# Performance work log

Hardware: AMD Instinct MI355X
Metric: run time of the kernel (lower is better)

Reference implementation:

```python
import jax, jax.numpy as jnp
import numpy as np

N, E, D_IN, D_OUT = 16384, 4096, 256, 256


def _leaky(v):
    return jnp.where(v > 0, v, 0.1 * v)


def setup_inputs() -> dict:
    key = jax.random.key(0)
    ks = jax.random.split(key, 8)
    x = jax.random.normal(ks[0], (N, D_IN), dtype=jnp.float32)
    # 0/1 incidence mask, float32 (as multiplied in the torch code)
    H_shape = jax.random.randint(ks[1], (N, E), 0, 2).astype(jnp.float32)
    w1 = jax.random.normal(ks[2], (D_IN, D_OUT), dtype=jnp.float32)
    w2 = jax.random.normal(ks[3], (D_OUT, D_OUT), dtype=jnp.float32)
    a1 = jax.random.normal(ks[4], (D_OUT, 1), dtype=jnp.float32)
    a21 = jax.random.normal(ks[5], (D_OUT, 1), dtype=jnp.float32)
    a22 = jax.random.normal(ks[6], (D_OUT, 1), dtype=jnp.float32)
    return {"x": x, "H_shape": H_shape, "w1": w1, "w2": w2,
            "a1": a1, "a21": a21, "a22": a22}


def reference(x, H_shape, w1, w2, a1, a21, a22):
    xw1 = x @ w1                                  # [N, D]
    # node->edge attention (masked softmax-like over nodes, axis -2)
    f = _leaky(xw1) @ a1                          # [N, 1]
    e = jnp.exp(jnp.tanh(f / 8) * 8) * H_shape    # [N, E]
    e = e / jnp.sum(e, axis=-2, keepdims=True)    # normalize over nodes
    # edge features
    f = _leaky(e.T @ xw1)                         # [E, D]
    # edge->node attention (masked normalize over edges, axis -1)
    b = (_leaky(f @ w2) @ a21).T + _leaky(xw1) @ a22  # [1,E] + [N,1] -> [N,E]
    b = jnp.exp(jnp.tanh(b / 8) * 8) * H_shape
    b = b / jnp.sum(b, axis=-1, keepdims=True)
    return _leaky(b @ f @ w2)                     # [N, D]
```

## Files before the change

### kernel.cpp

```cpp
#include <hip/hip_runtime.h>


typedef __attribute__((ext_vector_type(8))) short short8;
typedef __attribute__((ext_vector_type(4))) short short4v;
typedef __attribute__((ext_vector_type(4))) float f32x4;

__device__ __forceinline__ float leakyf(float v) { return v > 0.f ? v : 0.1f * v; }
__device__ __forceinline__ float fastrcp(float x) { return __builtin_amdgcn_rcpf(x); }

__device__ __forceinline__ float satexpf(float t) {
    float u = fminf(fmaxf(t * 0.25f, -30.f), 30.f);
    float p = __expf(u);
    float th = (p - 1.f) * fastrcp(p + 1.f);
    return __expf(8.f * th);
}

__device__ __forceinline__ short f2b(float v) {
    unsigned int x = __float_as_uint(v);
    x += 0x7fffu + ((x >> 16) & 1u);
    return (short)(x >> 16);
}
__device__ __forceinline__ float b2f(short s) {
    return __uint_as_float(((unsigned int)(unsigned short)s) << 16);
}

__global__ __launch_bounds__(256) void transpose_f32_bf16(
        const float* __restrict__ src, short* __restrict__ dst, int R, int C) {
    __shared__ float Ts[64][65];
    const int t = threadIdx.x;
    const long r0 = (long)blockIdx.x * 64;
    const long c0 = (long)blockIdx.y * 64;
    {
        const int row = t >> 2, cc = (t & 3) * 16;
        const float* p = src + (r0 + row) * (long)C + c0 + cc;
#pragma unroll
        for (int i = 0; i < 4; ++i) {
            f32x4 v = *reinterpret_cast<const f32x4*>(p + i * 4);
#pragma unroll
            for (int k = 0; k < 4; ++k) Ts[row][cc + i * 4 + k] = v[k];
        }
    }
    __syncthreads();
    {
        const int cl = t >> 2, ch = (t & 3) * 16;
        short8 pk0, pk1;
#pragma unroll
        for (int i = 0; i < 8; ++i) pk0[i] = f2b(Ts[ch + i][cl]);
#pragma unroll
        for (int i = 0; i < 8; ++i) pk1[i] = f2b(Ts[ch + 8 + i][cl]);
        short* q = dst + (c0 + cl) * (long)R + r0 + ch;
        *reinterpret_cast<short8*>(q) = pk0;
        *reinterpret_cast<short8*>(q + 8) = pk1;
    }
}

__global__ __launch_bounds__(256) void transpose_split(
        const float* __restrict__ src, short* __restrict__ dh,
        short* __restrict__ dl, int R, int C) {
    __shared__ float Ts[64][65];
    const int t = threadIdx.x;
    const long r0 = (long)blockIdx.x * 64;
    const long c0 = (long)blockIdx.y * 64;
    {
        const int row = t >> 2, cc = (t & 3) * 16;
        const float* p = src + (r0 + row) * (long)C + c0 + cc;
#pragma unroll
        for (int i = 0; i < 4; ++i) {
            f32x4 v = *reinterpret_cast<const f32x4*>(p + i * 4);
#pragma unroll
            for (int k = 0; k < 4; ++k) Ts[row][cc + i * 4 + k] = v[k];
        }
    }
    __syncthreads();
    {
        const int cl = t >> 2, ch = (t & 3) * 16;
        short8 h0, h1, l0, l1;
#pragma unroll
        for (int i = 0; i < 8; ++i) {
            float v = Ts[ch + i][cl];
            short h = f2b(v);
            h0[i] = h; l0[i] = f2b(v - b2f(h));
        }
#pragma unroll
        for (int i = 0; i < 8; ++i) {
            float v = Ts[ch + 8 + i][cl];
            short h = f2b(v);
            h1[i] = h; l1[i] = f2b(v - b2f(h));
        }
        short* qh = dh + (c0 + cl) * (long)R + r0 + ch;
        short* ql = dl + (c0 + cl) * (long)R + r0 + ch;
        *reinterpret_cast<short8*>(qh) = h0;
        *reinterpret_cast<short8*>(qh + 8) = h1;
        *reinterpret_cast<short8*>(ql) = l0;
        *reinterpret_cast<short8*>(ql + 8) = l1;
    }
}

__global__ __launch_bounds__(256) void gemm_xw1(
        const float* __restrict__ A, const short* __restrict__ Bh,
        const short* __restrict__ Bl, float* __restrict__ C) {
    __shared__ short Ash[128][72];
    __shared__ short Asl[128][72];
    __shared__ short Bsh[64][72];
    __shared__ short Bsl[64][72];
    const int t = threadIdx.x;
    const int wid = t >> 6, lane = t & 63;
    const int wm = wid & 1, wn = wid >> 1;
    const int quad = lane >> 4, l15 = lane & 15;
    const long m0 = (long)blockIdx.x * 128;
    const long n0 = (long)blockIdx.y * 64;
    f32x4 acc[4][2];
#pragma unroll
    for (int i = 0; i < 4; ++i)
#pragma unroll
        for (int j = 0; j < 2; ++j)
#pragma unroll
            for (int r = 0; r < 4; ++r) acc[i][j][r] = 0.f;

    for (int kb = 0; kb < 256; kb += 64) {
#pragma unroll
        for (int it = 0; it < 4; ++it) {
            const int cid = t + it * 256;
            const int row = cid >> 3, c8 = (cid & 7) * 8;
            const float* ap = A + (m0 + row) * 256 + kb + c8;
            f32x4 v0 = *reinterpret_cast<const f32x4*>(ap);
            f32x4 v1 = *reinterpret_cast<const f32x4*>(ap + 4);
            short8 hi, lo;
#pragma unroll
            for (int k = 0; k < 4; ++k) {
                short h0 = f2b(v0[k]); hi[k] = h0; lo[k] = f2b(v0[k] - b2f(h0));
                short h1 = f2b(v1[k]); hi[4 + k] = h1; lo[4 + k] = f2b(v1[k] - b2f(h1));
            }
            *reinterpret_cast<short8*>(&Ash[row][c8]) = hi;
            *reinterpret_cast<short8*>(&Asl[row][c8]) = lo;
        }
#pragma unroll
        for (int it = 0; it < 2; ++it) {
            const int cid = t + it * 256;
            const int row = cid >> 3, c8 = (cid & 7) * 8;
            *reinterpret_cast<short8*>(&Bsh[row][c8]) =
                *reinterpret_cast<const short8*>(Bh + (n0 + row) * 256 + kb + c8);
            *reinterpret_cast<short8*>(&Bsl[row][c8]) =
                *reinterpret_cast<const short8*>(Bl + (n0 + row) * 256 + kb + c8);
        }
        __syncthreads();
#pragma unroll
        for (int ks = 0; ks < 2; ++ks) {
            short8 ah[4], al[4], bh[2], bl[2];
#pragma unroll
            for (int i = 0; i < 4; ++i) {
                ah[i] = *reinterpret_cast<const short8*>(&Ash[wm * 64 + i * 16 + l15][ks * 32 + quad * 8]);
                al[i] = *reinterpret_cast<const short8*>(&Asl[wm * 64 + i * 16 + l15][ks * 32 + quad * 8]);
            }
#pragma unroll
            for (int j = 0; j < 2; ++j) {
                bh[j] = *reinterpret_cast<const short8*>(&Bsh[wn * 32 + j * 16 + l15][ks * 32 + quad * 8]);
                bl[j] = *reinterpret_cast<const short8*>(&Bsl[wn * 32 + j * 16 + l15][ks * 32 + quad * 8]);
            }
#pragma unroll
            for (int i = 0; i < 4; ++i)
#pragma unroll
                for (int j = 0; j < 2; ++j) {
                    acc[i][j] = __builtin_amdgcn_mfma_f32_16x16x32_bf16(ah[i], bh[j], acc[i][j], 0, 0, 0);
                    acc[i][j] = __builtin_amdgcn_mfma_f32_16x16x32_bf16(ah[i], bl[j], acc[i][j], 0, 0, 0);
                    acc[i][j] = __builtin_amdgcn_mfma_f32_16x16x32_bf16(al[i], bh[j], acc[i][j], 0, 0, 0);
                }
        }
        __syncthreads();
    }
#pragma unroll
    for (int i = 0; i < 4; ++i) {
        const long grow = m0 + wm * 64 + i * 16 + quad * 4;
#pragma unroll
        for (int j = 0; j < 2; ++j) {
            const long gcol = n0 + wn * 32 + j * 16 + l15;
#pragma unroll
            for (int r = 0; r < 4; ++r)
                C[(grow + r) * 256 + gcol] = acc[i][j][r];
        }
    }
}

__global__ __launch_bounds__(256) void node_stats(
        const float* __restrict__ xw1, const float* __restrict__ a1,
        const float* __restrict__ a22, short* __restrict__ yT,
        float* __restrict__ dn) {
    __shared__ short Ys[257][72];
    const int t = threadIdx.x;
    const int n0 = blockIdx.x * 64;
    const int r = t >> 2, q = t & 3;
    const long n = n0 + r;
    const float* xp = xw1 + n * 256 + q * 64;
    float vals[64];
    float facc = 0.f, dacc = 0.f;
#pragma unroll
    for (int i = 0; i < 16; ++i) {
        f32x4 v  = *reinterpret_cast<const f32x4*>(xp + i * 4);
        f32x4 b1 = *reinterpret_cast<const f32x4*>(a1 + q * 64 + i * 4);
        f32x4 b2 = *reinterpret_cast<const f32x4*>(a22 + q * 64 + i * 4);
#pragma unroll
        for (int k = 0; k < 4; ++k) {
            float lv = leakyf(v[k]);
            facc += lv * b1[k];
            dacc += lv * b2[k];
            vals[i * 4 + k] = v[k];
        }
    }
    facc += __shfl_xor(facc, 1); facc += __shfl_xor(facc, 2);
    dacc += __shfl_xor(dacc, 1); dacc += __shfl_xor(dacc, 2);
    const float g = satexpf(facc);
    const int dr = t >> 3, c8 = (t & 7) * 8;
    if (q == 0) { dn[n] = dacc; Ys[256][r] = f2b(g); }
#pragma unroll
    for (int i = 0; i < 64; ++i) Ys[q * 64 + i][r] = f2b(vals[i] * g);
    __syncthreads();
    for (int it = 0; it < 9; ++it) {
        const int d = it * 32 + dr;
        short8 pk;
        if (d <= 256) pk = *reinterpret_cast<const short8*>(&Ys[d][c8]);
        else { short8 z = {0,0,0,0,0,0,0,0}; pk = z; }
        *reinterpret_cast<short8*>(yT + (long)d * 16384 + n0 + c8) = pk;
    }
    __syncthreads();
    if (q == 0) Ys[256][r] = f2b(g - b2f(f2b(g)));
#pragma unroll
    for (int i = 0; i < 64; ++i) {
        float yv = vals[i] * g;
        Ys[q * 64 + i][r] = f2b(yv - b2f(f2b(yv)));
    }
    __syncthreads();
    for (int it = 0; it < 9; ++it) {
        const int d = it * 32 + dr;
        short8 pk;
        if (d <= 256) pk = *reinterpret_cast<const short8*>(&Ys[d][c8]);
        else { short8 z = {0,0,0,0,0,0,0,0}; pk = z; }
        *reinterpret_cast<short8*>(yT + (long)(288 + d) * 16384 + n0 + c8) = pk;
    }
}

template<int BM, int BN, int EPI>
__global__ __launch_bounds__(256) void gemm_bt(
        const short* __restrict__ Ab, const short* __restrict__ Bb,
        float* __restrict__ C, long ldA, long ldB, long ldC,
        int Ktile, const float* __restrict__ aux, long zstrideC) {
    constexpr int BK = 64;
    constexpr int TM = BM / 32, TN = BN / 32;
    __shared__ short As[BM][BK + 8];
    __shared__ short Bs[BN][BK + 8];
    const int t = threadIdx.x;
    const int wid = t >> 6, lane = t & 63;
    const int wm = wid & 1, wn = wid >> 1;
    const int quad = lane >> 4, l15 = lane & 15;
    const long m0 = (long)blockIdx.x * BM;
    const long n0 = (long)blockIdx.y * BN;
    const long k0 = (long)blockIdx.z * Ktile;
    float* Cz = C + (long)blockIdx.z * zstrideC;

    f32x4 acc[TM][TN];
#pragma unroll
    for (int i = 0; i < TM; ++i)
#pragma unroll
        for (int j = 0; j < TN; ++j)
#pragma unroll
            for (int r = 0; r < 4; ++r) acc[i][j][r] = 0.f;

    for (int kb = 0; kb < Ktile; kb += BK) {
#pragma unroll
        for (int it = 0; it < BM * BK / 2048; ++it) {
            const int cid = t + it * 256;
            const int row = cid >> 3, c8 = (cid & 7) * 8;
            *reinterpret_cast<short8*>(&As[row][c8]) =
                *reinterpret_cast<const short8*>(Ab + (m0 + row) * ldA + k0 + kb + c8);
        }
#pragma unroll
        for (int it = 0; it < BN * BK / 2048; ++it) {
            const int cid = t + it * 256;
            const int row = cid >> 3, c8 = (cid & 7) * 8;
            *reinterpret_cast<short8*>(&Bs[row][c8]) =
                *reinterpret_cast<const short8*>(Bb + (n0 + row) * ldB + k0 + kb + c8);
        }
        __syncthreads();
#pragma unroll
        for (int ks = 0; ks < 2; ++ks) {
            short8 af[TM], bf[TN];
#pragma unroll
            for (int i = 0; i < TM; ++i)
                af[i] = *reinterpret_cast<const short8*>(
                        &As[wm * (BM / 2) + i * 16 + l15][ks * 32 + quad * 8]);
#pragma unroll
            for (int j = 0; j < TN; ++j)
                bf[j] = *reinterpret_cast<const short8*>(
                        &Bs[wn * (BN / 2) + j * 16 + l15][ks * 32 + quad * 8]);
#pragma unroll
            for (int i = 0; i < TM; ++i)
#pragma unroll
                for (int j = 0; j < TN; ++j)
                    acc[i][j] = __builtin_amdgcn_mfma_f32_16x16x32_bf16(
                            af[i], bf[j], acc[i][j], 0, 0, 0);
        }
        __syncthreads();
    }
#pragma unroll
    for (int i = 0; i < TM; ++i) {
        const long grow = m0 + wm * (BM / 2) + i * 16 + quad * 4;
#pragma unroll
        for (int j = 0; j < TN; ++j) {
            const long gcol = n0 + wn * (BN / 2) + j * 16 + l15;
#pragma unroll
            for (int r = 0; r < 4; ++r) {
                const float v = acc[i][j][r];
                float* cp = Cz + (grow + r) * ldC + gcol;
                if (EPI == 0) *cp = v;
                else *cp = leakyf(v * fastrcp(aux[grow + r]));
            }
        }
    }
}

__global__ __launch_bounds__(256) void reduce_C1(
        const float* __restrict__ C1p, float* __restrict__ C1) {
    const int i = blockIdx.x * 256 + threadIdx.x;
    const int j = i / 288, dd = i - j * 288;
    const float* p = C1p + (long)j * 576 + dd;
    float s = 0.f;
#pragma unroll
    for (int z = 0; z < 4; ++z) {
        const float* pz = p + (long)z * 4096 * 576;
        s += pz[0] + pz[288];
    }
    C1[i] = s;
}

__global__ __launch_bounds__(256) void gemm_G(
        const float* __restrict__ C1, const short* __restrict__ w2Th,
        const short* __restrict__ w2Tl, const float* __restrict__ a21,
        short* __restrict__ GT, float* __restrict__ cat) {
    __shared__ short Ash[64][72];
    __shared__ short Asl[64][72];
    __shared__ short Bsh[64][72];
    __shared__ short Bsl[64][72];
    __shared__ float Gs[64][65];
    const int t = threadIdx.x;
    const int wid = t >> 6, lane = t & 63;
    const int wm = wid & 1, wn = wid >> 1;
    const int quad = lane >> 4, l15 = lane & 15;
    const long j0 = (long)blockIdx.x * 64;
    const long d0 = (long)blockIdx.y * 64;
    f32x4 acc[2][2];
#pragma unroll
    for (int i = 0; i < 2; ++i)
#pragma unroll
        for (int j = 0; j < 2; ++j)
#pragma unroll
            for (int r = 0; r < 4; ++r) acc[i][j][r] = 0.f;

    for (int kb = 0; kb < 256; kb += 64) {
#pragma unroll
        for (int it = 0; it < 2; ++it) {
            const int cid = t + it * 256;
            const int row = cid >> 3, c8 = (cid & 7) * 8;
            const float rd = fastrcp(C1[(j0 + row) * 288 + 256]);
            const float* ap = C1 + (j0 + row) * 288 + kb + c8;
            f32x4 v0 = *reinterpret_cast<const f32x4*>(ap);
            f32x4 v1 = *reinterpret_cast<const f32x4*>(ap + 4);
            short8 hi, lo;
#pragma unroll
            for (int k = 0; k < 4; ++k) {
                float f0 = leakyf(v0[k] * rd);
                float f1 = leakyf(v1[k] * rd);
                short h0 = f2b(f0); hi[k] = h0; lo[k] = f2b(f0 - b2f(h0));
                short h1 = f2b(f1); hi[4 + k] = h1; lo[4 + k] = f2b(f1 - b2f(h1));
            }
            *reinterpret_cast<short8*>(&Ash[row][c8]) = hi;
            *reinterpret_cast<short8*>(&Asl[row][c8]) = lo;
            *reinterpret_cast<short8*>(&Bsh[row][c8]) =
                *reinterpret_cast<const short8*>(w2Th + (d0 + row) * 256 + kb + c8);
            *reinterpret_cast<short8*>(&Bsl[row][c8]) =
                *reinterpret_cast<const short8*>(w2Tl + (d0 + row) * 256 + kb + c8);
        }
        __syncthreads();
#pragma unroll
        for (int ks = 0; ks < 2; ++ks) {
            short8 ah[2], al[2], bh[2], bl[2];
#pragma unroll
            for (int i = 0; i < 2; ++i) {
                ah[i] = *reinterpret_cast<const short8*>(&Ash[wm * 32 + i * 16 + l15][ks * 32 + quad * 8]);
                al[i] = *reinterpret_cast<const short8*>(&Asl[wm * 32 + i * 16 + l15][ks * 32 + quad * 8]);
            }
#pragma unroll
            for (int j = 0; j < 2; ++j) {
                bh[j] = *reinterpret_cast<const short8*>(&Bsh[wn * 32 + j * 16 + l15][ks * 32 + quad * 8]);
                bl[j] = *reinterpret_cast<const short8*>(&Bsl[wn * 32 + j * 16 + l15][ks * 32 + quad * 8]);
            }
#pragma unroll
            for (int i = 0; i < 2; ++i)
#pragma unroll
                for (int j = 0; j < 2; ++j) {
                    acc[i][j] = __builtin_amdgcn_mfma_f32_16x16x32_bf16(ah[i], bh[j], acc[i][j], 0, 0, 0);
                    acc[i][j] = __builtin_amdgcn_mfma_f32_16x16x32_bf16(ah[i], bl[j], acc[i][j], 0, 0, 0);
                    acc[i][j] = __builtin_amdgcn_mfma_f32_16x16x32_bf16(al[i], bh[j], acc[i][j], 0, 0, 0);
                }
        }
        __syncthreads();
    }
#pragma unroll
    for (int i = 0; i < 2; ++i)
#pragma unroll
        for (int j = 0; j < 2; ++j)
#pragma unroll
            for (int r = 0; r < 4; ++r)
                Gs[wm * 32 + i * 16 + quad * 4 + r][wn * 32 + j * 16 + l15] = acc[i][j][r];
    __syncthreads();
    {
        const int jl = t >> 2, q = t & 3;
        float cp = 0.f;
#pragma unroll
        for (int i = 0; i < 16; ++i) {
            const int d = q * 16 + i;
            cp += leakyf(Gs[jl][d]) * a21[d0 + d];
        }
        cp += __shfl_xor(cp, 1); cp += __shfl_xor(cp, 2);
        if (q == 0) atomicAdd(&cat[j0 + jl], cp);
    }
    {
        const int dl = t >> 2, q = t & 3;
        short8 pk0, pk1;
#pragma unroll
        for (int i = 0; i < 8; ++i) pk0[i] = f2b(Gs[q * 16 + i][dl]);
#pragma unroll
        for (int i = 0; i < 8; ++i) pk1[i] = f2b(Gs[q * 16 + 8 + i][dl]);
        short* gp = GT + (d0 + dl) * 4096 + j0 + q * 16;
        *reinterpret_cast<short8*>(gp) = pk0;
        *reinterpret_cast<short8*>(gp + 8) = pk1;
    }
}

__global__ __launch_bounds__(256) void edge_weights(
        const float* __restrict__ H, const float* __restrict__ cat,
        const float* __restrict__ dn, short* __restrict__ Bmat,
        float* __restrict__ rsum) {
    const long n = blockIdx.x;
    const int t = threadIdx.x;
    const float dv = dn[n];
    const float* hp = H + n * 4096;
    short* bp = Bmat + n * 4096;
    float acc = 0.f;
#pragma unroll
    for (int c = 0; c < 4; ++c) {
        const int j = c * 1024 + t * 4;
        f32x4 h  = *reinterpret_cast<const f32x4*>(hp + j);
        f32x4 cv = *reinterpret_cast<const f32x4*>(cat + j);
        short4v pk;
#pragma unroll
        for (int k = 0; k < 4; ++k) {
            const float s = satexpf(cv[k] + dv) * h[k];
            const short sb = f2b(s);
            pk[k] = sb;
            acc += b2f(sb);
        }
        *reinterpret_cast<short4v*>(bp + j) = pk;
    }
#pragma unroll
    for (int m = 1; m < 64; m <<= 1) acc += __shfl_xor(acc, m);
    __shared__ float wsum[4];
    if ((t & 63) == 0) wsum[t >> 6] = acc;
    __syncthreads();
    if (t == 0) rsum[n] = wsum[0] + wsum[1] + wsum[2] + wsum[3];
}

extern "C" void kernel_launch(void* const* d_in, const int* in_sizes, int n_in,
                              void* d_out, int out_size, void* d_ws, size_t ws_size,
                              hipStream_t stream) {
    const float* x   = (const float*)d_in[0];
    const float* H   = (const float*)d_in[1];
    const float* w1  = (const float*)d_in[2];
    const float* w2  = (const float*)d_in[3];
    const float* a1  = (const float*)d_in[4];
    const float* a21 = (const float*)d_in[5];
    const float* a22 = (const float*)d_in[6];
    float* out = (float*)d_out;
    char* ws = (char*)d_ws;

    float* xw1  = (float*)(ws + 0);
    float* C1p  = (float*)(ws + 0);
    short* yT   = (short*)(ws + 37748736);
    float* dn   = (float*)(ws + 56623104);
    short* w1Th = (short*)(ws + 56688640);
    short* w1Tl = (short*)(ws + 56819712);
    short* w2Th = (short*)(ws + 56950784);
    short* w2Tl = (short*)(ws + 57081856);
    float* C1   = (float*)(ws + 57212928);
    short* GT   = (short*)(ws + 61931520);
    float* cat  = (float*)(ws + 64028672);
    float* rsum = (float*)(ws + 64045056);
    short* HbT  = (short*)(ws + 64110592);
    short* Bmat = HbT;

    transpose_split<<<dim3(4, 4), 256, 0, stream>>>(w1, w1Th, w1Tl, 256, 256);
    transpose_split<<<dim3(4, 4), 256, 0, stream>>>(w2, w2Th, w2Tl, 256, 256);
    transpose_f32_bf16<<<dim3(256, 64), 256, 0, stream>>>(H, HbT, 16384, 4096);

    gemm_xw1<<<dim3(128, 4), 256, 0, stream>>>(x, w1Th, w1Tl, xw1);

    node_stats<<<dim3(256), 256, 0, stream>>>(xw1, a1, a22, yT, dn);

    gemm_bt<128, 96, 0><<<dim3(32, 6, 4), 256, 0, stream>>>(
            HbT, yT, C1p, 16384, 16384, 576, 4096, nullptr, (long)4096 * 576);
    reduce_C1<<<dim3(4608), 256, 0, stream>>>(C1p, C1);

    hipMemsetAsync(cat, 0, 4096 * sizeof(float), stream);
    gemm_G<<<dim3(64, 4), 256, 0, stream>>>(C1, w2Th, w2Tl, a21, GT, cat);

    edge_weights<<<dim3(16384), 256, 0, stream>>>(H, cat, dn, Bmat, rsum);

    gemm_bt<128, 64, 2><<<dim3(128, 4, 1), 256, 0, stream>>>(
            Bmat, GT, out, 4096, 4096, 256, 4096, rsum, 0);
}
```

Measured before the change: 727.0 us.

## Quantize H·Y GEMM to int8 split hi/lo with per-column scaling, bit-pack H mask

Replaces the bf16 hi/lo split H^T·Y GEMM with an int8 MFMA GEMM. H is exact as an int8 0/1 mask, and Y is quantized into two int8 halves of a 16-bit fixed-point value using per-column max scales gathered with atomicMax. H is also packed into a bitmask so edge_weights reads 1 bit instead of one fp32 per element. The final GEMM moves to a dedicated kernel with a 64x128 tile. This halves operand bytes for the largest GEMM and removes a second full read of H, at the cost of an extra quantization pass, scale atomics, and fixed-point precision loss.

New measurement: 673.3 us. -7.4%, faster.

```diff
diff --git a/kernel.cpp b/kernel.cpp
--- a/kernel.cpp
+++ b/kernel.cpp
@@ -2,8 +2,9 @@
 
 
 typedef __attribute__((ext_vector_type(8))) short short8;
-typedef __attribute__((ext_vector_type(4))) short short4v;
 typedef __attribute__((ext_vector_type(4))) float f32x4;
+typedef __attribute__((ext_vector_type(4))) int int4v;
+typedef __attribute__((ext_vector_type(4))) unsigned int uint4v;
 
 __device__ __forceinline__ float leakyf(float v) { return v > 0.f ? v : 0.1f * v; }
 __device__ __forceinline__ float fastrcp(float x) { return __builtin_amdgcn_rcpf(x); }
@@ -22,36 +23,6 @@
 }
 __device__ __forceinline__ float b2f(short s) {
     return __uint_as_float(((unsigned int)(unsigned short)s) << 16);
-}
-
-__global__ __launch_bounds__(256) void transpose_f32_bf16(
-        const float* __restrict__ src, short* __restrict__ dst, int R, int C) {
-    __shared__ float Ts[64][65];
-    const int t = threadIdx.x;
-    const long r0 = (long)blockIdx.x * 64;
-    const long c0 = (long)blockIdx.y * 64;
-    {
-        const int row = t >> 2, cc = (t & 3) * 16;
-        const float* p = src + (r0 + row) * (long)C + c0 + cc;
-#pragma unroll
-        for (int i = 0; i < 4; ++i) {
-            f32x4 v = *reinterpret_cast<const f32x4*>(p + i * 4);
-#pragma unroll
-            for (int k = 0; k < 4; ++k) Ts[row][cc + i * 4 + k] = v[k];
-        }
-    }
-    __syncthreads();
-    {
-        const int cl = t >> 2, ch = (t & 3) * 16;
-        short8 pk0, pk1;
-#pragma unroll
-        for (int i = 0; i < 8; ++i) pk0[i] = f2b(Ts[ch + i][cl]);
-#pragma unroll
-        for (int i = 0; i < 8; ++i) pk1[i] = f2b(Ts[ch + 8 + i][cl]);
-        short* q = dst + (c0 + cl) * (long)R + r0 + ch;
-        *reinterpret_cast<short8*>(q) = pk0;
-        *reinterpret_cast<short8*>(q + 8) = pk1;
-    }
 }
 
 __global__ __launch_bounds__(256) void transpose_split(
@@ -93,6 +64,47 @@
         *reinterpret_cast<short8*>(qh + 8) = h1;
         *reinterpret_cast<short8*>(ql) = l0;
         *reinterpret_cast<short8*>(ql + 8) = l1;
+    }
+}
+
+__global__ __launch_bounds__(256) void transposeH_pack(
+        const float* __restrict__ H, char* __restrict__ HbT,
+        unsigned int* __restrict__ Hbits) {
+    __shared__ float Ts[64][65];
+    const int t = threadIdx.x;
+    const long r0 = (long)blockIdx.x * 64;
+    const long c0 = (long)blockIdx.y * 64;
+    {
+        const int row = t >> 2, cc = (t & 3) * 16;
+        const float* p = H + (r0 + row) * 4096L + c0 + cc;
+#pragma unroll
+        for (int i = 0; i < 4; ++i) {
+            f32x4 v = *reinterpret_cast<const f32x4*>(p + i * 4);
+#pragma unroll
+            for (int k = 0; k < 4; ++k) Ts[row][cc + i * 4 + k] = v[k];
+        }
+    }
+    __syncthreads();
+    {
+        const int cl = t >> 2, ch = (t & 3) * 16;
+        uint4v pk;
+#pragma unroll
+        for (int wv = 0; wv < 4; ++wv) {
+            unsigned int u = 0;
+#pragma unroll
+            for (int b = 0; b < 4; ++b)
+                u |= (Ts[ch + wv * 4 + b][cl] != 0.f ? 1u : 0u) << (8 * b);
+            pk[wv] = u;
+        }
+        *reinterpret_cast<uint4v*>(HbT + (c0 + cl) * 16384L + r0 + ch) = pk;
+    }
+    if (t < 128) {
+        const int nl = t >> 1, w = t & 1;
+        unsigned int u = 0;
+#pragma unroll
+        for (int b = 0; b < 32; ++b)
+            u |= (Ts[nl][w * 32 + b] != 0.f ? 1u : 0u) << b;
+        Hbits[(r0 + nl) * 128 + (c0 >> 5) + w] = u;
     }
 }
 
@@ -181,11 +193,11 @@
     }
 }
 
-__global__ __launch_bounds__(256) void node_stats(
+__global__ __launch_bounds__(256) void node_stats1(
         const float* __restrict__ xw1, const float* __restrict__ a1,
-        const float* __restrict__ a22, short* __restrict__ yT,
-        float* __restrict__ dn) {
-    __shared__ short Ys[257][72];
+        const float* __restrict__ a22, float* __restrict__ g_out,
+        float* __restrict__ dn, unsigned int* __restrict__ ddmax) {
+    __shared__ float Mx[4][260];
     const int t = threadIdx.x;
     const int n0 = blockIdx.x * 64;
     const int r = t >> 2, q = t & 3;
@@ -209,126 +221,190 @@
     facc += __shfl_xor(facc, 1); facc += __shfl_xor(facc, 2);
     dacc += __shfl_xor(dacc, 1); dacc += __shfl_xor(dacc, 2);
     const float g = satexpf(facc);
-    const int dr = t >> 3, c8 = (t & 7) * 8;
-    if (q == 0) { dn[n] = dacc; Ys[256][r] = f2b(g); }
-#pragma unroll
-    for (int i = 0; i < 64; ++i) Ys[q * 64 + i][r] = f2b(vals[i] * g);
+    if (q == 0) { dn[n] = dacc; g_out[n] = g; }
+    float lm[64];
+#pragma unroll
+    for (int i = 0; i < 64; ++i) lm[i] = fabsf(vals[i] * g);
+#pragma unroll
+    for (int m = 4; m < 64; m <<= 1)
+#pragma unroll
+        for (int i = 0; i < 64; ++i) lm[i] = fmaxf(lm[i], __shfl_xor(lm[i], m));
+    float gm = g;
+#pragma unroll
+    for (int m = 1; m < 64; m <<= 1) gm = fmaxf(gm, __shfl_xor(gm, m));
+    const int wv = t >> 6, lane = t & 63;
+    if (lane < 4) {
+#pragma unroll
+        for (int i = 0; i < 64; ++i) Mx[wv][lane * 64 + i] = lm[i];
+    }
+    if (lane == 0) Mx[wv][256] = gm;
     __syncthreads();
-    for (int it = 0; it < 9; ++it) {
-        const int d = it * 32 + dr;
-        short8 pk;
-        if (d <= 256) pk = *reinterpret_cast<const short8*>(&Ys[d][c8]);
-        else { short8 z = {0,0,0,0,0,0,0,0}; pk = z; }
-        *reinterpret_cast<short8*>(yT + (long)d * 16384 + n0 + c8) = pk;
-    }
+    if (t < 256) {
+        float m = fmaxf(fmaxf(Mx[0][t], Mx[1][t]), fmaxf(Mx[2][t], Mx[3][t]));
+        atomicMax(&ddmax[t], __float_as_uint(m));
+    }
+    if (t == 0) {
+        float m = fmaxf(fmaxf(Mx[0][256], Mx[1][256]), fmaxf(Mx[2][256], Mx[3][256]));
+        atomicMax(&ddmax[256], __float_as_uint(m));
+    }
+}
+
+__global__ __launch_bounds__(256) void quantize_y(
+        const float* __restrict__ xw1, const float* __restrict__ g_in,
+        const unsigned int* __restrict__ ddmax, char* __restrict__ yQ) {
+    __shared__ unsigned int Qh[257][16];
+    __shared__ unsigned int Ql[257][16];
+    const int t = threadIdx.x;
+    const int n0 = blockIdx.x * 64;
+    const int dd0 = (t >> 4) * 16;
+    const int w = t & 15;
+    const int r4 = w * 4;
+    float s[16];
+#pragma unroll
+    for (int i = 0; i < 16; ++i)
+        s[i] = 32512.f / __uint_as_float(ddmax[dd0 + i]);
+    const float sg = 32512.f / __uint_as_float(ddmax[256]);
+    unsigned int bh[16], bl[16];
+#pragma unroll
+    for (int i = 0; i < 16; ++i) { bh[i] = 0u; bl[i] = 0u; }
+    unsigned int gh = 0u, gl = 0u;
+#pragma unroll
+    for (int rr = 0; rr < 4; ++rr) {
+        const long n = n0 + r4 + rr;
+        const float gg = g_in[n];
+        const float* xp = xw1 + n * 256 + dd0;
+#pragma unroll
+        for (int c = 0; c < 4; ++c) {
+            f32x4 v = *reinterpret_cast<const f32x4*>(xp + c * 4);
+#pragma unroll
+            for (int k = 0; k < 4; ++k) {
+                const int i = c * 4 + k;
+                int qv = __float2int_rn(v[k] * gg * s[i]);
+                qv = max(-32639, min(32639, qv));
+                const int qh = (qv + 128) >> 8;
+                const int ql = qv - (qh << 8);
+                bh[i] |= ((unsigned int)(qh & 255)) << (8 * rr);
+                bl[i] |= ((unsigned int)(ql & 255)) << (8 * rr);
+            }
+        }
+        if (t < 16) {
+            int qv = __float2int_rn(gg * sg);
+            qv = max(-32639, min(32639, qv));
+            const int qh = (qv + 128) >> 8;
+            const int ql = qv - (qh << 8);
+            gh |= ((unsigned int)(qh & 255)) << (8 * rr);
+            gl |= ((unsigned int)(ql & 255)) << (8 * rr);
+        }
+    }
+#pragma unroll
+    for (int i = 0; i < 16; ++i) { Qh[dd0 + i][w] = bh[i]; Ql[dd0 + i][w] = bl[i]; }
+    if (t < 16) { Qh[256][t] = gh; Ql[256][t] = gl; }
     __syncthreads();
-    if (q == 0) Ys[256][r] = f2b(g - b2f(f2b(g)));
-#pragma unroll
-    for (int i = 0; i < 64; ++i) {
-        float yv = vals[i] * g;
-        Ys[q * 64 + i][r] = f2b(yv - b2f(f2b(yv)));
-    }
-    __syncthreads();
-    for (int it = 0; it < 9; ++it) {
-        const int d = it * 32 + dr;
-        short8 pk;
-        if (d <= 256) pk = *reinterpret_cast<const short8*>(&Ys[d][c8]);
-        else { short8 z = {0,0,0,0,0,0,0,0}; pk = z; }
-        *reinterpret_cast<short8*>(yT + (long)(288 + d) * 16384 + n0 + c8) = pk;
-    }
-}
-
-template<int BM, int BN, int EPI>
-__global__ __launch_bounds__(256) void gemm_bt(
-        const short* __restrict__ Ab, const short* __restrict__ Bb,
-        float* __restrict__ C, long ldA, long ldB, long ldC,
-        int Ktile, const float* __restrict__ aux, long zstrideC) {
-    constexpr int BK = 64;
-    constexpr int TM = BM / 32, TN = BN / 32;
-    __shared__ short As[BM][BK + 8];
-    __shared__ short Bs[BN][BK + 8];
+#pragma unroll
+    for (int it = 0; it < 2; ++it) {
+        const int dd = it * 256 + t;
+        if (dd < 288) {
+#pragma unroll
+            for (int s2 = 0; s2 < 4; ++s2) {
+                uint4v vh, vl;
+                if (dd < 257) {
+                    vh = *reinterpret_cast<const uint4v*>(&Qh[dd][s2 * 4]);
+                    vl = *reinterpret_cast<const uint4v*>(&Ql[dd][s2 * 4]);
+                } else {
+#pragma unroll
+                    for (int k = 0; k < 4; ++k) { vh[k] = 0u; vl[k] = 0u; }
+                }
+                *reinterpret_cast<uint4v*>(yQ + (long)dd * 16384 + n0 + s2 * 16) = vh;
+                *reinterpret_cast<uint4v*>(yQ + (long)(288 + dd) * 16384 + n0 + s2 * 16) = vl;
+            }
+        }
+    }
+}
+
+__global__ __launch_bounds__(256) void gemm_c1_i8(
+        const char* __restrict__ Ab, const char* __restrict__ Bb,
+        int* __restrict__ Cp) {
+    __shared__ char As[128][144];
+    __shared__ char Bs[96][144];
     const int t = threadIdx.x;
     const int wid = t >> 6, lane = t & 63;
     const int wm = wid & 1, wn = wid >> 1;
     const int quad = lane >> 4, l15 = lane & 15;
-    const long m0 = (long)blockIdx.x * BM;
-    const long n0 = (long)blockIdx.y * BN;
-    const long k0 = (long)blockIdx.z * Ktile;
-    float* Cz = C + (long)blockIdx.z * zstrideC;
-
-    f32x4 acc[TM][TN];
-#pragma unroll
-    for (int i = 0; i < TM; ++i)
-#pragma unroll
-        for (int j = 0; j < TN; ++j)
-#pragma unroll
-            for (int r = 0; r < 4; ++r) acc[i][j][r] = 0.f;
-
-    for (int kb = 0; kb < Ktile; kb += BK) {
-#pragma unroll
-        for (int it = 0; it < BM * BK / 2048; ++it) {
+    const long m0 = (long)blockIdx.x * 128;
+    const long n0 = (long)blockIdx.y * 96;
+    const long k0 = (long)blockIdx.z * 4096;
+    int* Cz = Cp + (long)blockIdx.z * (4096L * 576);
+    int4v acc[4][3];
+#pragma unroll
+    for (int i = 0; i < 4; ++i)
+#pragma unroll
+        for (int j = 0; j < 3; ++j)
+#pragma unroll
+            for (int r = 0; r < 4; ++r) acc[i][j][r] = 0;
+
+    for (int kb = 0; kb < 4096; kb += 128) {
+#pragma unroll
+        for (int it = 0; it < 4; ++it) {
             const int cid = t + it * 256;
-            const int row = cid >> 3, c8 = (cid & 7) * 8;
-            *reinterpret_cast<short8*>(&As[row][c8]) =
-                *reinterpret_cast<const short8*>(Ab + (m0 + row) * ldA + k0 + kb + c8);
-        }
-#pragma unroll
-        for (int it = 0; it < BN * BK / 2048; ++it) {
+            const int row = cid >> 3, seg = (cid & 7) * 16;
+            *reinterpret_cast<uint4v*>(&As[row][seg]) =
+                *reinterpret_cast<const uint4v*>(Ab + (m0 + row) * 16384 + k0 + kb + seg);
+        }
+#pragma unroll
+        for (int it = 0; it < 3; ++it) {
             const int cid = t + it * 256;
-            const int row = cid >> 3, c8 = (cid & 7) * 8;
-            *reinterpret_cast<short8*>(&Bs[row][c8]) =
-                *reinterpret_cast<const short8*>(Bb + (n0 + row) * ldB + k0 + kb + c8);
+            const int row = cid >> 3, seg = (cid & 7) * 16;
+            *reinterpret_cast<uint4v*>(&Bs[row][seg]) =
+                *reinterpret_cast<const uint4v*>(Bb + (n0 + row) * 16384 + k0 + kb + seg);
         }
         __syncthreads();
 #pragma unroll
         for (int ks = 0; ks < 2; ++ks) {
-            short8 af[TM], bf[TN];
-#pragma unroll
-            for (int i = 0; i < TM; ++i)
-                af[i] = *reinterpret_cast<const short8*>(
-                        &As[wm * (BM / 2) + i * 16 + l15][ks * 32 + quad * 8]);
-#pragma unroll
-            for (int j = 0; j < TN; ++j)
-                bf[j] = *reinterpret_cast<const short8*>(
-                        &Bs[wn * (BN / 2) + j * 16 + l15][ks * 32 + quad * 8]);
-#pragma unroll
-            for (int i = 0; i < TM; ++i)
-#pragma unroll
-                for (int j = 0; j < TN; ++j)
-                    acc[i][j] = __builtin_amdgcn_mfma_f32_16x16x32_bf16(
+            int4v af[4], bf[3];
+#pragma unroll
+            for (int i = 0; i < 4; ++i)
+                af[i] = *reinterpret_cast<const int4v*>(
+                        &As[wm * 64 + i * 16 + l15][ks * 64 + quad * 16]);
+#pragma unroll
+            for (int j = 0; j < 3; ++j)
+                bf[j] = *reinterpret_cast<const int4v*>(
+                        &Bs[wn * 48 + j * 16 + l15][ks * 64 + quad * 16]);
+#pragma unroll
+            for (int i = 0; i < 4; ++i)
+#pragma unroll
+                for (int j = 0; j < 3; ++j)
+                    acc[i][j] = __builtin_amdgcn_mfma_i32_16x16x64_i8(
                             af[i], bf[j], acc[i][j], 0, 0, 0);
         }
         __syncthreads();
     }
 #pragma unroll
-    for (int i = 0; i < TM; ++i) {
-        const long grow = m0 + wm * (BM / 2) + i * 16 + quad * 4;
-#pragma unroll
-        for (int j = 0; j < TN; ++j) {
-            const long gcol = n0 + wn * (BN / 2) + j * 16 + l15;
-#pragma unroll
-            for (int r = 0; r < 4; ++r) {
-                const float v = acc[i][j][r];
-                float* cp = Cz + (grow + r) * ldC + gcol;
-                if (EPI == 0) *cp = v;
-                else *cp = leakyf(v * fastrcp(aux[grow + r]));
-            }
+    for (int i = 0; i < 4; ++i) {
+        const long grow = m0 + wm * 64 + i * 16 + quad * 4;
+#pragma unroll
+        for (int j = 0; j < 3; ++j) {
+            const long gcol = n0 + wn * 48 + j * 16 + l15;
+#pragma unroll
+            for (int r = 0; r < 4; ++r)
+                Cz[(grow + r) * 576 + gcol] = acc[i][j][r];
         }
     }
 }
 
 __global__ __launch_bounds__(256) void reduce_C1(
-        const float* __restrict__ C1p, float* __restrict__ C1) {
+        const int* __restrict__ C1p, const unsigned int* __restrict__ ddmax,
+        float* __restrict__ C1) {
     const int i = blockIdx.x * 256 + threadIdx.x;
     const int j = i / 288, dd = i - j * 288;
-    const float* p = C1p + (long)j * 576 + dd;
-    float s = 0.f;
+    const int* p = C1p + (long)j * 576 + dd;
+    int sh = 0, sl = 0;
 #pragma unroll
     for (int z = 0; z < 4; ++z) {
-        const float* pz = p + (long)z * 4096 * 576;
-        s += pz[0] + pz[288];
-    }
-    C1[i] = s;
+        const int* pz = p + (long)z * 4096 * 576;
+        sh += pz[0]; sl += pz[288];
+    }
+    const float scale = __uint_as_float(ddmax[dd]) * (1.f / 32512.f);
+    C1[i] = (float)(sh * 256 + sl) * scale;
 }
 
 __global__ __launch_bounds__(256) void gemm_G(
@@ -436,36 +512,109 @@
 }
 
 __global__ __launch_bounds__(256) void edge_weights(
-        const float* __restrict__ H, const float* __restrict__ cat,
+        const unsigned int* __restrict__ Hbits, const float* __restrict__ cat,
         const float* __restrict__ dn, short* __restrict__ Bmat,
         float* __restrict__ rsum) {
     const long n = blockIdx.x;
     const int t = threadIdx.x;
     const float dv = dn[n];
-    const float* hp = H + n * 4096;
-    short* bp = Bmat + n * 4096;
+    const unsigned int w = Hbits[n * 128 + (t >> 1)];
+    const int bo = (t & 1) * 16;
+    short* bp = Bmat + n * 4096 + t * 16;
     float acc = 0.f;
+    short8 pk0, pk1;
 #pragma unroll
     for (int c = 0; c < 4; ++c) {
-        const int j = c * 1024 + t * 4;
-        f32x4 h  = *reinterpret_cast<const f32x4*>(hp + j);
-        f32x4 cv = *reinterpret_cast<const f32x4*>(cat + j);
-        short4v pk;
+        f32x4 cv = *reinterpret_cast<const f32x4*>(cat + t * 16 + c * 4);
 #pragma unroll
         for (int k = 0; k < 4; ++k) {
-            const float s = satexpf(cv[k] + dv) * h[k];
+            const int kk = c * 4 + k;
+            const float s = ((w >> (bo + kk)) & 1u) ? satexpf(cv[k] + dv) : 0.f;
             const short sb = f2b(s);
-            pk[k] = sb;
+            if (kk < 8) pk0[kk] = sb; else pk1[kk - 8] = sb;
             acc += b2f(sb);
         }
-        *reinterpret_cast<short4v*>(bp + j) = pk;
-    }
+    }
+    *reinterpret_cast<short8*>(bp) = pk0;
+    *reinterpret_cast<short8*>(bp + 8) = pk1;
 #pragma unroll
     for (int m = 1; m < 64; m <<= 1) acc += __shfl_xor(acc, m);
     __shared__ float wsum[4];
     if ((t & 63) == 0) wsum[t >> 6] = acc;
     __syncthreads();
     if (t == 0) rsum[n] = wsum[0] + wsum[1] + wsum[2] + wsum[3];
+}
+
+template<int BM, int BN>
+__global__ __launch_bounds__(256) void gemm_final(
+        const short* __restrict__ Ab, const short* __restrict__ Bb,
+        float* __restrict__ C, const float* __restrict__ aux) {
+    constexpr int BK = 64;
+    constexpr int TM = BM / 32, TN = BN / 32;
+    __shared__ short As[BM][BK + 8];
+    __shared__ short Bs[BN][BK + 8];
+    const int t = threadIdx.x;
+    const int wid = t >> 6, lane = t & 63;
+    const int wm = wid & 1, wn = wid >> 1;
+    const int quad = lane >> 4, l15 = lane & 15;
+    const long m0 = (long)blockIdx.x * BM;
+    const long n0 = (long)blockIdx.y * BN;
+    f32x4 acc[TM][TN];
+#pragma unroll
+    for (int i = 0; i < TM; ++i)
+#pragma unroll
+        for (int j = 0; j < TN; ++j)
+#pragma unroll
+            for (int r = 0; r < 4; ++r) acc[i][j][r] = 0.f;
+
+    for (int kb = 0; kb < 4096; kb += BK) {
+#pragma unroll
+        for (int it = 0; it < BM * BK / 2048; ++it) {
+            const int cid = t + it * 256;
+            const int row = cid >> 3, c8 = (cid & 7) * 8;
+            *reinterpret_cast<short8*>(&As[row][c8]) =
+                *reinterpret_cast<const short8*>(Ab + (m0 + row) * 4096 + kb + c8);
+        }
+#pragma unroll
+        for (int it = 0; it < BN * BK / 2048; ++it) {
+            const int cid = t + it * 256;
+            const int row = cid >> 3, c8 = (cid & 7) * 8;
+            *reinterpret_cast<short8*>(&Bs[row][c8]) =
+                *reinterpret_cast<const short8*>(Bb + (n0 + row) * 4096 + kb + c8);
+        }
+        __syncthreads();
+#pragma unroll
+        for (int ks = 0; ks < 2; ++ks) {
+            short8 af[TM], bf[TN];
+#pragma unroll
+            for (int i = 0; i < TM; ++i)
+                af[i] = *reinterpret_cast<const short8*>(
+                        &As[wm * (BM / 2) + i * 16 + l15][ks * 32 + quad * 8]);
+#pragma unroll
+            for (int j = 0; j < TN; ++j)
+                bf[j] = *reinterpret_cast<const short8*>(
+                        &Bs[wn * (BN / 2) + j * 16 + l15][ks * 32 + quad * 8]);
+#pragma unroll
+            for (int i = 0; i < TM; ++i)
+#pragma unroll
+                for (int j = 0; j < TN; ++j)
+                    acc[i][j] = __builtin_amdgcn_mfma_f32_16x16x32_bf16(
+                            af[i], bf[j], acc[i][j], 0, 0, 0);
+        }
+        __syncthreads();
+    }
+#pragma unroll
+    for (int i = 0; i < TM; ++i) {
+        const long grow = m0 + wm * (BM / 2) + i * 16 + quad * 4;
+#pragma unroll
+        for (int j = 0; j < TN; ++j) {
+            const long gcol = n0 + wn * (BN / 2) + j * 16 + l15;
+#pragma unroll
+            for (int r = 0; r < 4; ++r)
+                C[(grow + r) * 256 + gcol] =
+                    leakyf(acc[i][j][r] * fastrcp(aux[grow + r]));
+        }
+    }
 }
 
 extern "C" void kernel_launch(void* const* d_in, const int* in_sizes, int n_in,
@@ -481,38 +630,41 @@
     float* out = (float*)d_out;
     char* ws = (char*)d_ws;
 
-    float* xw1  = (float*)(ws + 0);
-    float* C1p  = (float*)(ws + 0);
-    short* yT   = (short*)(ws + 37748736);
-    float* dn   = (float*)(ws + 56623104);
-    short* w1Th = (short*)(ws + 56688640);
-    short* w1Tl = (short*)(ws + 56819712);
-    short* w2Th = (short*)(ws + 56950784);
-    short* w2Tl = (short*)(ws + 57081856);
-    float* C1   = (float*)(ws + 57212928);
-    short* GT   = (short*)(ws + 61931520);
-    float* cat  = (float*)(ws + 64028672);
-    float* rsum = (float*)(ws + 64045056);
-    short* HbT  = (short*)(ws + 64110592);
-    short* Bmat = HbT;
+    float* xw1   = (float*)(ws + 0);
+    int*   C1p   = (int*)(ws + 0);
+    short* Bmat  = (short*)(ws + 0);
+    char*  HbT   = (char*)(ws + 67108864);
+    char*  yQ    = (char*)(ws + 134217728);
+    float* dn    = (float*)(ws + 143654912);
+    float* g     = (float*)(ws + 143720448);
+    unsigned int* ddmax = (unsigned int*)(ws + 143785984);
+    short* w1Th  = (short*)(ws + 143790080);
+    short* w1Tl  = (short*)(ws + 143921152);
+    short* w2Th  = (short*)(ws + 144052224);
+    short* w2Tl  = (short*)(ws + 144183296);
+    float* C1    = (float*)(ws + 144314368);
+    short* GT    = (short*)(ws + 149032960);
+    float* cat   = (float*)(ws + 151130112);
+    float* rsum  = (float*)(ws + 151146496);
+    unsigned int* Hbits = (unsigned int*)(ws + 151212032);
+
+    hipMemsetAsync(ddmax, 0, 288 * sizeof(unsigned int), stream);
+    hipMemsetAsync(cat, 0, 4096 * sizeof(float), stream);
 
     transpose_split<<<dim3(4, 4), 256, 0, stream>>>(w1, w1Th, w1Tl, 256, 256);
     transpose_split<<<dim3(4, 4), 256, 0, stream>>>(w2, w2Th, w2Tl, 256, 256);
-    transpose_f32_bf16<<<dim3(256, 64), 256, 0, stream>>>(H, HbT, 16384, 4096);
+    transposeH_pack<<<dim3(256, 64), 256, 0, stream>>>(H, HbT, Hbits);
 
     gemm_xw1<<<dim3(128, 4), 256, 0, stream>>>(x, w1Th, w1Tl, xw1);
-
-    node_stats<<<dim3(256), 256, 0, stream>>>(xw1, a1, a22, yT, dn);
-
-    gemm_bt<128, 96, 0><<<dim3(32, 6, 4), 256, 0, stream>>>(
-            HbT, yT, C1p, 16384, 16384, 576, 4096, nullptr, (long)4096 * 576);
-    reduce_C1<<<dim3(4608), 256, 0, stream>>>(C1p, C1);
-
-    hipMemsetAsync(cat, 0, 4096 * sizeof(float), stream);
+    node_stats1<<<dim3(256), 256, 0, stream>>>(xw1, a1, a22, g, dn, ddmax);
+    quantize_y<<<dim3(256), 256, 0, stream>>>(xw1, g, ddmax, yQ);
+
+    gemm_c1_i8<<<dim3(32, 6, 4), 256, 0, stream>>>(HbT, yQ, C1p);
+    reduce_C1<<<dim3(4608), 256, 0, stream>>>(C1p, ddmax, C1);
+
     gemm_G<<<dim3(64, 4), 256, 0, stream>>>(C1, w2Th, w2Tl, a21, GT, cat);
 
-    edge_weights<<<dim3(16384), 256, 0, stream>>>(H, cat, dn, Bmat, rsum);
-
-    gemm_bt<128, 64, 2><<<dim3(128, 4, 1), 256, 0, stream>>>(
-            Bmat, GT, out, 4096, 4096, 256, 4096, rsum, 0);
-}
+    edge_weights<<<dim3(16384), 256, 0, stream>>>(Hbits, cat, dn, Bmat, rsum);
+
+    gemm_final<64, 128><<<dim3(256, 2), 256, 0, stream>>>(Bmat, GT, out, rsum);
+}
```
